# Kernel tuning notes

Hardware: AMD Instinct MI355X
Metric: run time of the kernel (lower is better)

The kernel has to match this reference:

```python
import jax, jax.numpy as jnp
import numpy as np

B, T, SLATE, D = 256, 16, 20, 256
N_ITEMS, N_USERS = 100000, 10000


def setup_inputs() -> dict:
    key = jax.random.key(0)
    ks = jax.random.split(key, 8)
    s = 1.0 / np.sqrt(D)  # PyTorch GRU/Linear init scale ~ U(-1/sqrt(H), 1/sqrt(H))
    return {
        "item_idxs": jax.random.randint(ks[0], (B, T, SLATE), 0, N_ITEMS),
        "user_idxs": jax.random.randint(ks[1], (B, T), 0, N_USERS),
        "responses": jnp.zeros((B, T, SLATE), jnp.float32),
        "item_table": jax.random.normal(ks[2], (N_ITEMS, D), jnp.float32) * 0.02,
        "user_table": jax.random.normal(ks[3], (N_USERS, D), jnp.float32) * 0.02,
        "W_ih": jax.random.uniform(ks[4], (3 * D, 2 * D), jnp.float32, -s, s),
        "W_hh": jax.random.uniform(ks[5], (3 * D, D), jnp.float32, -s, s),
        "b_ih": jnp.zeros((3 * D,), jnp.float32),
        "b_hh": jnp.zeros((3 * D,), jnp.float32),
        "W_out": jax.random.uniform(ks[6], (1, D), jnp.float32, -s, s),
        "b_out": jnp.zeros((1,), jnp.float32),
    }


def _gru_cell(x, h, W_ih, W_hh, b_ih, b_hh):
    # PyTorch GRUCell math. x: [N, 2D], h: [N, D]
    gi = x @ W_ih.T + b_ih  # [N, 3D]
    gh = h @ W_hh.T + b_hh  # [N, 3D]
    i_r, i_z, i_n = jnp.split(gi, 3, axis=-1)
    h_r, h_z, h_n = jnp.split(gh, 3, axis=-1)
    r = jax.nn.sigmoid(i_r + h_r)
    z = jax.nn.sigmoid(i_z + h_z)
    n = jnp.tanh(i_n + r * h_n)
    return (1.0 - z) * n + z * h


def reference(item_idxs, user_idxs, responses, item_table, user_table,
              W_ih, W_hh, b_ih, b_hh, W_out, b_out):
    # embedding lookup: item_embs [B,T,S,D], user_embs [B,T,D]
    item_embs = item_table[item_idxs]
    user_embs = user_table[user_idxs]
    N = B * T
    e = item_embs.reshape(N, SLATE, D).transpose(1, 0, 2)  # [S, N, D]
    h0 = user_embs.reshape(N, D)
    m0 = jnp.ones((N, 1), item_embs.dtype)  # 'soft' readout multiplier, 1 at step 0

    def step(carry, e_i):
        h, m = carry
        x = jnp.concatenate([e_i, e_i * m], axis=-1)  # [N, 2D]
        h = _gru_cell(x, h, W_ih, W_hh, b_ih, b_hh)
        y = h @ W_out.T + b_out  # [N, 1]
        return (h, jax.nn.sigmoid(y)), y[:, 0]

    _, ys = jax.lax.scan(step, (h0, m0), e)  # ys: [S, N]
    return ys.transpose(1, 0).reshape(B, T, SLATE)
```

## Files before the change

### kernel.cpp

```cpp
#include <hip/hip_runtime.h>
#include <math.h>

#define SLATE 20
#define DD 256
#define NSEQ 4096

typedef __attribute__((ext_vector_type(8))) short bf16x8;
typedef __attribute__((ext_vector_type(4))) float f32x4;
typedef unsigned short u16;
typedef unsigned int u32;

__device__ __forceinline__ u16 f2bf(float f) {
    unsigned u = __float_as_uint(f);
    u += 0x7fff + ((u >> 16) & 1);
    return (u16)(u >> 16);
}
__device__ __forceinline__ float blo(u32 u) { return __uint_as_float(u << 16); }
__device__ __forceinline__ float bhi(u32 u) { return __uint_as_float(u & 0xffff0000u); }
__device__ __forceinline__ float sigm_(float x) {
    return __builtin_amdgcn_rcpf(1.f + __builtin_amdgcn_exp2f(-1.44269504f * x));
}
__device__ __forceinline__ float tanh_(float x) {
    return 1.f - 2.f * __builtin_amdgcn_rcpf(1.f + __builtin_amdgcn_exp2f(2.88539008f * x));
}

__device__ __forceinline__ void gl_lds16(const void* g, void* l) {
    __builtin_amdgcn_global_load_lds(
        (const __attribute__((address_space(1))) unsigned int*)g,
        (__attribute__((address_space(3))) unsigned int*)l, 16, 0, 0);
}

__global__ void prep_w(const float* __restrict__ W_ih, const float* __restrict__ W_hh,
                       u16* __restrict__ W12, u16* __restrict__ Whh) {
    int i = blockIdx.x * 256 + threadIdx.x;
    if (i < 1536 * 256) {
        int j = i >> 8, k = i & 255;
        float v = (j < 768) ? W_ih[(size_t)j * 512 + k]
                            : W_ih[(size_t)(j - 768) * 512 + 256 + k];
        W12[i] = f2bf(v);
    } else {
        int i2 = i - 1536 * 256;
        Whh[i2] = f2bf(W_hh[i2]);
    }
}

__global__ void gather_e(int s0, const int* __restrict__ idxs, const float* __restrict__ itab,
                         u16* __restrict__ e_bf) {
    int g = blockIdx.x * 256 + threadIdx.x;
    int row = g >> 6, c = g & 63;
    int n = row & (NSEQ - 1), s = s0 + (row >> 12);
    int idx = idxs[n * SLATE + s];
    float4 v = *(const float4*)&itab[(size_t)idx * DD + c * 4];
    ushort4 o;
    o.x = f2bf(v.x); o.y = f2bf(v.y); o.z = f2bf(v.z); o.w = f2bf(v.w);
    *(ushort4*)&e_bf[(size_t)row * DD + c * 4] = o;
}

__global__ __launch_bounds__(256) void gemm_e(
        const u16* __restrict__ e_bf, const u16* __restrict__ W12,
        const float* __restrict__ b_ih, u16* __restrict__ Ge) {
    __shared__ u16 A_s[128][32];
    __shared__ u16 B_s[128][32];

    const int tid = threadIdx.x;
    const int w = tid >> 6, l = tid & 63, lm = l & 15, lq = l >> 4;
    const int wm = w & 1, wn = w >> 1;
    const size_t m0 = (size_t)blockIdx.y * 128;
    const size_t n0 = (size_t)blockIdx.x * 128;

    f32x4 acc[4][4];
    f32x4 zero4 = {0.f, 0.f, 0.f, 0.f};
#pragma unroll
    for (int mi = 0; mi < 4; ++mi)
#pragma unroll
        for (int nj = 0; nj < 4; ++nj) acc[mi][nj] = zero4;

    const int srow = w * 16 + (l >> 2);
    const int skc = (l & 3) * 8;
    const u16* gA = e_bf + (m0 + srow) * DD + skc;
    const u16* gB = W12 + (n0 + srow) * DD + skc;
    u16* lA = &A_s[0][0] + w * 512 + l * 8;
    u16* lB = &B_s[0][0] + w * 512 + l * 8;

    for (int kt = 0; kt < 8; ++kt) {
        const int ko = kt * 32;
        gl_lds16(gA + ko, lA);
        gl_lds16(gA + 64 * DD + ko, lA + 2048);
        gl_lds16(gB + ko, lB);
        gl_lds16(gB + 64 * DD + ko, lB + 2048);
        __syncthreads();
        bf16x8 af[4], bfr[4];
#pragma unroll
        for (int mi = 0; mi < 4; ++mi)
            af[mi] = *(const bf16x8*)&A_s[wm * 64 + mi * 16 + lm][lq * 8];
#pragma unroll
        for (int nj = 0; nj < 4; ++nj)
            bfr[nj] = *(const bf16x8*)&B_s[wn * 64 + nj * 16 + lm][lq * 8];
#pragma unroll
        for (int nj = 0; nj < 4; ++nj)
#pragma unroll
            for (int mi = 0; mi < 4; ++mi)
                acc[mi][nj] = __builtin_amdgcn_mfma_f32_16x16x32_bf16(af[mi], bfr[nj], acc[mi][nj], 0, 0, 0);
        __syncthreads();
    }
    float bb[4];
#pragma unroll
    for (int nj = 0; nj < 4; ++nj) {
        int col = (int)n0 + wn * 64 + nj * 16 + lm;
        bb[nj] = (col < 768) ? b_ih[col] : 0.f;
    }
#pragma unroll
    for (int mi = 0; mi < 4; ++mi)
#pragma unroll
        for (int rr = 0; rr < 4; ++rr) {
            u16* gp = Ge + (m0 + wm * 64 + mi * 16 + lq * 4 + rr) * 1536 + n0 + wn * 64 + lm;
#pragma unroll
            for (int nj = 0; nj < 4; ++nj) gp[nj * 16] = f2bf(acc[mi][nj][rr] + bb[nj]);
        }
}

__device__ __forceinline__ int hA_off(int seq, int kt, int lq2) {
    int v = ((kt & 3) << 2) | lq2;
    return kt * 512 + lq2 * 128 + ((seq ^ v) << 3);
}

__global__ __launch_bounds__(1024, 4) void seq_kernel(
        int s0, int C,
        const u16* __restrict__ Ge,
        const u16* __restrict__ Whh,
        const int* __restrict__ user_idxs, const float* __restrict__ user_table,
        const float* __restrict__ b_hh,
        const float* __restrict__ W_out, const float* __restrict__ b_out,
        float* __restrict__ h_g, float* __restrict__ m_g, float* __restrict__ out)
{
    __shared__ u16   hA[4096];
    __shared__ float gh_s[16][770];
    __shared__ u16   geL[2][16][1536];

    const int tid = threadIdx.x;
    const int w = tid >> 6, l = tid & 63, lm = l & 15, lq = l >> 4;
    const int n0 = blockIdx.x * 16;
    const int nw = n0 + w;
    const int jw = w * 48;

    const u16* wbase = Whh + (size_t)(jw + lm) * DD + lq * 8;
    bf16x8 warr0[8], warr1[8];
#pragma unroll
    for (int kt = 0; kt < 8; ++kt) {
        warr0[kt] = *(const bf16x8*)(wbase + kt * 32);
        warr1[kt] = *(const bf16x8*)(wbase + 16 * DD + kt * 32);
    }
    const u16* wb2 = wbase + 32 * DD;

    float bhh0 = b_hh[jw + lm], bhh1 = b_hh[jw + 16 + lm], bhh2 = b_hh[jw + 32 + lm];
    float2 woA = *(const float2*)&W_out[2 * l];
    float2 woB = *(const float2*)&W_out[2 * l + 128];
    const float bo = b_out[0];

    float h_reg[4]; float m_w;
    if (s0 == 0) {
        const float* hu = user_table + (size_t)user_idxs[nw] * DD;
        float2 a = *(const float2*)&hu[2 * l];
        float2 b = *(const float2*)&hu[2 * l + 128];
        h_reg[0] = a.x; h_reg[1] = a.y; h_reg[2] = b.x; h_reg[3] = b.y; m_w = 1.f;
    } else {
        float2 a = *(const float2*)&h_g[(size_t)nw * DD + 2 * l];
        float2 b = *(const float2*)&h_g[(size_t)nw * DD + 2 * l + 128];
        h_reg[0] = a.x; h_reg[1] = a.y; h_reg[2] = b.x; h_reg[3] = b.y; m_w = m_g[nw];
    }
#pragma unroll
    for (int c = 0; c < 2; ++c) {
        int kt = (l >> 4) + 4 * c, lq2 = (l >> 2) & 3;
        u32 pk = (u32)f2bf(h_reg[2 * c]) | ((u32)f2bf(h_reg[2 * c + 1]) << 16);
        *(u32*)&hA[hA_off(w, kt, lq2) + 2 * (l & 3)] = pk;
    }

    {
        const u16* g0 = Ge + ((size_t)0 * NSEQ + n0) * 1536;
        u16* l0 = &geL[0][0][0];
#pragma unroll
        for (int i = 0; i < 3; ++i) {
            int ii = w + 16 * i;
            gl_lds16(g0 + ii * 512 + l * 8, l0 + ii * 512);
        }
    }
    asm volatile("s_waitcnt lgkmcnt(0)" ::: "memory");
    __builtin_amdgcn_s_barrier();
    __builtin_amdgcn_sched_barrier(0);

    for (int sc = 0; sc < C; ++sc) {
        const int cur = sc & 1;

        f32x4 zero4 = {0.f, 0.f, 0.f, 0.f};
        f32x4 acc0 = zero4, acc1 = zero4, acc2 = zero4;
#pragma unroll
        for (int kt = 0; kt < 8; ++kt) {
            bf16x8 af = *(const bf16x8*)&hA[hA_off(lm, kt, lq)];
            acc0 = __builtin_amdgcn_mfma_f32_16x16x32_bf16(af, warr0[kt], acc0, 0, 0, 0);
            acc1 = __builtin_amdgcn_mfma_f32_16x16x32_bf16(af, warr1[kt], acc1, 0, 0, 0);
            bf16x8 b2 = *(const bf16x8*)(wb2 + kt * 32);
            acc2 = __builtin_amdgcn_mfma_f32_16x16x32_bf16(af, b2, acc2, 0, 0, 0);
        }

        __builtin_amdgcn_sched_barrier(0);
        if (sc + 1 < C) {
            const u16* gnx = Ge + ((size_t)(sc + 1) * NSEQ + n0) * 1536;
            u16* lnx = &geL[cur ^ 1][0][0];
#pragma unroll
            for (int i = 0; i < 3; ++i) {
                int ii = w + 16 * i;
                gl_lds16(gnx + ii * 512 + l * 8, lnx + ii * 512);
            }
        }

#pragma unroll
        for (int rr = 0; rr < 4; ++rr) {
            gh_s[lq * 4 + rr][jw + lm]      = acc0[rr] + bhh0;
            gh_s[lq * 4 + rr][jw + 16 + lm] = acc1[rr] + bhh1;
            gh_s[lq * 4 + rr][jw + 32 + lm] = acc2[rr] + bhh2;
        }
        asm volatile("s_waitcnt vmcnt(3) lgkmcnt(0)" ::: "memory");
        __builtin_amdgcn_s_barrier();
        __builtin_amdgcn_sched_barrier(0);

        const u32* grow = (const u32*)&geL[cur][w][0];
        u32 ge2[2][6];
#pragma unroll
        for (int c = 0; c < 2; ++c)
#pragma unroll
            for (int g = 0; g < 6; ++g)
                ge2[c][g] = grow[g * 128 + 64 * c + l];

        float yv = 0.f;
#pragma unroll
        for (int c = 0; c < 2; ++c) {
            const int d0 = 2 * l + 128 * c;
            float2 ghr = *(const float2*)&gh_s[w][d0];
            float2 ghz = *(const float2*)&gh_s[w][256 + d0];
            float2 ghn = *(const float2*)&gh_s[w][512 + d0];
            float ir_lo = fmaf(m_w, blo(ge2[c][3]), blo(ge2[c][0]));
            float ir_hi = fmaf(m_w, bhi(ge2[c][3]), bhi(ge2[c][0]));
            float iz_lo = fmaf(m_w, blo(ge2[c][4]), blo(ge2[c][1]));
            float iz_hi = fmaf(m_w, bhi(ge2[c][4]), bhi(ge2[c][1]));
            float in_lo = fmaf(m_w, blo(ge2[c][5]), blo(ge2[c][2]));
            float in_hi = fmaf(m_w, bhi(ge2[c][5]), bhi(ge2[c][2]));
            float r_lo = sigm_(ir_lo + ghr.x);
            float r_hi = sigm_(ir_hi + ghr.y);
            float z_lo = sigm_(iz_lo + ghz.x);
            float z_hi = sigm_(iz_hi + ghz.y);
            float n_lo = tanh_(fmaf(r_lo, ghn.x, in_lo));
            float n_hi = tanh_(fmaf(r_hi, ghn.y, in_hi));
            float hn_lo = fmaf(z_lo, h_reg[2 * c] - n_lo, n_lo);
            float hn_hi = fmaf(z_hi, h_reg[2 * c + 1] - n_hi, n_hi);
            h_reg[2 * c] = hn_lo; h_reg[2 * c + 1] = hn_hi;
            int kt = (l >> 4) + 4 * c, lq2 = (l >> 2) & 3;
            u32 pk = (u32)f2bf(hn_lo) | ((u32)f2bf(hn_hi) << 16);
            *(u32*)&hA[hA_off(w, kt, lq2) + 2 * (l & 3)] = pk;
            float2 wo2 = c ? woB : woA;
            yv += hn_lo * wo2.x + hn_hi * wo2.y;
        }
#pragma unroll
        for (int off = 32; off > 0; off >>= 1) yv += __shfl_xor(yv, off, 64);
        float y = yv + bo;
        if (l == 0) out[(size_t)nw * SLATE + (s0 + sc)] = y;
        m_w = sigm_(y);

        asm volatile("s_waitcnt lgkmcnt(0)" ::: "memory");
        __builtin_amdgcn_s_barrier();
        __builtin_amdgcn_sched_barrier(0);
    }

#pragma unroll
    for (int c = 0; c < 2; ++c) {
        float2 v; v.x = h_reg[2 * c]; v.y = h_reg[2 * c + 1];
        *(float2*)&h_g[(size_t)nw * DD + 2 * l + 128 * c] = v;
    }
    if (l == 0) m_g[nw] = m_w;
}

extern "C" void kernel_launch(void* const* d_in, const int* in_sizes, int n_in,
                              void* d_out, int out_size, void* d_ws, size_t ws_size,
                              hipStream_t stream) {
    const int*   item_idxs  = (const int*)d_in[0];
    const int*   user_idxs  = (const int*)d_in[1];
    const float* item_table = (const float*)d_in[3];
    const float* user_table = (const float*)d_in[4];
    const float* W_ih       = (const float*)d_in[5];
    const float* W_hh       = (const float*)d_in[6];
    const float* b_ih       = (const float*)d_in[7];
    const float* b_hh       = (const float*)d_in[8];
    const float* W_out      = (const float*)d_in[9];
    const float* b_out      = (const float*)d_in[10];
    float* out = (float*)d_out;

    const size_t fixed = 786432ull + 393216ull + 4194304ull + 16384ull;
    static const int cands[5] = {10, 5, 4, 2, 1};
    int C = 1;
    for (int i = 0; i < 5; ++i) {
        size_t need = (size_t)cands[i] * (12582912ull + 2097152ull) + fixed;
        if (need <= ws_size) { C = cands[i]; break; }
    }

    u16*   Ge   = (u16*)d_ws;
    u16*   e_bf = (u16*)((char*)d_ws + (size_t)C * 12582912ull);
    u16*   W12  = (u16*)((char*)e_bf + (size_t)C * 2097152ull);
    u16*   Whh  = (u16*)((char*)W12 + 786432ull);
    float* h_g  = (float*)((char*)Whh + 393216ull);
    float* m_g  = (float*)((char*)h_g + 4194304ull);

    prep_w<<<2304, 256, 0, stream>>>(W_ih, W_hh, W12, Whh);

    for (int s0 = 0; s0 < SLATE; s0 += C) {
        gather_e<<<C * 1024, 256, 0, stream>>>(s0, item_idxs, item_table, e_bf);
        dim3 gg(12, 32 * C);
        gemm_e<<<gg, 256, 0, stream>>>(e_bf, W12, b_ih, Ge);
        seq_kernel<<<256, 1024, 0, stream>>>(s0, C, Ge, Whh, user_idxs, user_table,
                                             b_hh, W_out, b_out, h_g, m_g, out);
    }
}
```

Baseline: 445.8 us.

## Halve seq_kernel block size, keep all W_hh fragments in registers, fold b_hh

The recurrent kernel now uses 512 threads, 8 waves, with each wave computing 96 gate columns and holding all six W_hh fragments in registers. Previously one third of W_hh was re-read from global memory every step. Each wave now processes two sequences using half-wave lanes, and the r/z parts of b_hh are folded into the precomputed input GEMM bias. The next-step Ge prefetch is issued earlier, before the MFMAs. The cost is much higher register pressure, about 192 VGPRs for weights, and fewer waves for the per-step elementwise work.

```diff
diff --git a/kernel.cpp b/kernel.cpp
--- a/kernel.cpp
+++ b/kernel.cpp
@@ -58,7 +58,8 @@
 
 __global__ __launch_bounds__(256) void gemm_e(
         const u16* __restrict__ e_bf, const u16* __restrict__ W12,
-        const float* __restrict__ b_ih, u16* __restrict__ Ge) {
+        const float* __restrict__ b_ih, const float* __restrict__ b_hh,
+        u16* __restrict__ Ge) {
     __shared__ u16 A_s[128][32];
     __shared__ u16 B_s[128][32];
 
@@ -107,7 +108,8 @@
 #pragma unroll
     for (int nj = 0; nj < 4; ++nj) {
         int col = (int)n0 + wn * 64 + nj * 16 + lm;
-        bb[nj] = (col < 768) ? b_ih[col] : 0.f;
+        bb[nj] = 0.f;
+        if (col < 768) bb[nj] = b_ih[col] + (col < 512 ? b_hh[col] : 0.f);
     }
 #pragma unroll
     for (int mi = 0; mi < 4; ++mi)
@@ -124,7 +126,7 @@
     return kt * 512 + lq2 * 128 + ((seq ^ v) << 3);
 }
 
-__global__ __launch_bounds__(1024, 4) void seq_kernel(
+__global__ __launch_bounds__(512, 2) void seq_kernel(
         int s0, int C,
         const u16* __restrict__ Ge,
         const u16* __restrict__ Whh,
@@ -139,50 +141,66 @@
 
     const int tid = threadIdx.x;
     const int w = tid >> 6, l = tid & 63, lm = l & 15, lq = l >> 4;
+    const int l5 = l & 31, sh = l >> 5;
     const int n0 = blockIdx.x * 16;
-    const int nw = n0 + w;
-    const int jw = w * 48;
-
-    const u16* wbase = Whh + (size_t)(jw + lm) * DD + lq * 8;
-    bf16x8 warr0[8], warr1[8];
-#pragma unroll
-    for (int kt = 0; kt < 8; ++kt) {
-        warr0[kt] = *(const bf16x8*)(wbase + kt * 32);
-        warr1[kt] = *(const bf16x8*)(wbase + 16 * DD + kt * 32);
-    }
-    const u16* wb2 = wbase + 32 * DD;
-
-    float bhh0 = b_hh[jw + lm], bhh1 = b_hh[jw + 16 + lm], bhh2 = b_hh[jw + 32 + lm];
-    float2 woA = *(const float2*)&W_out[2 * l];
-    float2 woB = *(const float2*)&W_out[2 * l + 128];
+    const int sloc = 2 * w + sh;
+    const int nw = n0 + sloc;
+    const int jw2 = w * 96;
+
+    bf16x8 warr[6][8];
+    const u16* wb = Whh + (size_t)(jw2 + lm) * DD + lq * 8;
+#pragma unroll
+    for (int fi = 0; fi < 6; ++fi)
+#pragma unroll
+        for (int kt = 0; kt < 8; ++kt)
+            warr[fi][kt] = *(const bf16x8*)(wb + fi * 16 * DD + kt * 32);
+
+    float bn[6];
+#pragma unroll
+    for (int fi = 0; fi < 6; ++fi) {
+        int colb = jw2 + fi * 16;
+        bn[fi] = (colb >= 512) ? b_hh[colb + lm] : 0.f;
+    }
+
+    float wo[8];
+#pragma unroll
+    for (int j = 0; j < 4; ++j) {
+        float2 t = *(const float2*)&W_out[2 * l5 + 64 * j];
+        wo[2 * j] = t.x; wo[2 * j + 1] = t.y;
+    }
     const float bo = b_out[0];
 
-    float h_reg[4]; float m_w;
+    float h_reg[8]; float m_w;
     if (s0 == 0) {
         const float* hu = user_table + (size_t)user_idxs[nw] * DD;
-        float2 a = *(const float2*)&hu[2 * l];
-        float2 b = *(const float2*)&hu[2 * l + 128];
-        h_reg[0] = a.x; h_reg[1] = a.y; h_reg[2] = b.x; h_reg[3] = b.y; m_w = 1.f;
+#pragma unroll
+        for (int j = 0; j < 4; ++j) {
+            float2 t = *(const float2*)&hu[2 * l5 + 64 * j];
+            h_reg[2 * j] = t.x; h_reg[2 * j + 1] = t.y;
+        }
+        m_w = 1.f;
     } else {
-        float2 a = *(const float2*)&h_g[(size_t)nw * DD + 2 * l];
-        float2 b = *(const float2*)&h_g[(size_t)nw * DD + 2 * l + 128];
-        h_reg[0] = a.x; h_reg[1] = a.y; h_reg[2] = b.x; h_reg[3] = b.y; m_w = m_g[nw];
-    }
-#pragma unroll
-    for (int c = 0; c < 2; ++c) {
-        int kt = (l >> 4) + 4 * c, lq2 = (l >> 2) & 3;
-        u32 pk = (u32)f2bf(h_reg[2 * c]) | ((u32)f2bf(h_reg[2 * c + 1]) << 16);
-        *(u32*)&hA[hA_off(w, kt, lq2) + 2 * (l & 3)] = pk;
+        const float* hp = h_g + (size_t)nw * DD;
+#pragma unroll
+        for (int j = 0; j < 4; ++j) {
+            float2 t = *(const float2*)&hp[2 * l5 + 64 * j];
+            h_reg[2 * j] = t.x; h_reg[2 * j + 1] = t.y;
+        }
+        m_w = m_g[nw];
+    }
+#pragma unroll
+    for (int j = 0; j < 4; ++j) {
+        int ktw = (l5 >> 4) + 2 * j, lq2 = (l5 & 15) >> 2;
+        u32 pk = (u32)f2bf(h_reg[2 * j]) | ((u32)f2bf(h_reg[2 * j + 1]) << 16);
+        *(u32*)&hA[hA_off(sloc, ktw, lq2) + 2 * (l5 & 3)] = pk;
     }
 
     {
-        const u16* g0 = Ge + ((size_t)0 * NSEQ + n0) * 1536;
+        const u16* g0 = Ge + (size_t)n0 * 1536;
         u16* l0 = &geL[0][0][0];
 #pragma unroll
-        for (int i = 0; i < 3; ++i) {
-            int ii = w + 16 * i;
-            gl_lds16(g0 + ii * 512 + l * 8, l0 + ii * 512);
-        }
+        for (int i = 0; i < 6; ++i)
+            gl_lds16(g0 + tid * 8 + i * 4096, l0 + tid * 8 + i * 4096);
     }
     asm volatile("s_waitcnt lgkmcnt(0)" ::: "memory");
     __builtin_amdgcn_s_barrier();
@@ -191,78 +209,75 @@
     for (int sc = 0; sc < C; ++sc) {
         const int cur = sc & 1;
 
+        if (sc + 1 < C) {
+            const u16* gn = Ge + ((size_t)(sc + 1) * NSEQ + n0) * 1536;
+            u16* ln = &geL[cur ^ 1][0][0];
+#pragma unroll
+            for (int i = 0; i < 6; ++i)
+                gl_lds16(gn + tid * 8 + i * 4096, ln + tid * 8 + i * 4096);
+        }
+        __builtin_amdgcn_sched_barrier(0);
+
         f32x4 zero4 = {0.f, 0.f, 0.f, 0.f};
-        f32x4 acc0 = zero4, acc1 = zero4, acc2 = zero4;
+        f32x4 acc[6];
+#pragma unroll
+        for (int fi = 0; fi < 6; ++fi) acc[fi] = zero4;
 #pragma unroll
         for (int kt = 0; kt < 8; ++kt) {
             bf16x8 af = *(const bf16x8*)&hA[hA_off(lm, kt, lq)];
-            acc0 = __builtin_amdgcn_mfma_f32_16x16x32_bf16(af, warr0[kt], acc0, 0, 0, 0);
-            acc1 = __builtin_amdgcn_mfma_f32_16x16x32_bf16(af, warr1[kt], acc1, 0, 0, 0);
-            bf16x8 b2 = *(const bf16x8*)(wb2 + kt * 32);
-            acc2 = __builtin_amdgcn_mfma_f32_16x16x32_bf16(af, b2, acc2, 0, 0, 0);
-        }
-
-        __builtin_amdgcn_sched_barrier(0);
-        if (sc + 1 < C) {
-            const u16* gnx = Ge + ((size_t)(sc + 1) * NSEQ + n0) * 1536;
-            u16* lnx = &geL[cur ^ 1][0][0];
-#pragma unroll
-            for (int i = 0; i < 3; ++i) {
-                int ii = w + 16 * i;
-                gl_lds16(gnx + ii * 512 + l * 8, lnx + ii * 512);
-            }
-        }
-
-#pragma unroll
-        for (int rr = 0; rr < 4; ++rr) {
-            gh_s[lq * 4 + rr][jw + lm]      = acc0[rr] + bhh0;
-            gh_s[lq * 4 + rr][jw + 16 + lm] = acc1[rr] + bhh1;
-            gh_s[lq * 4 + rr][jw + 32 + lm] = acc2[rr] + bhh2;
-        }
-        asm volatile("s_waitcnt vmcnt(3) lgkmcnt(0)" ::: "memory");
+#pragma unroll
+            for (int fi = 0; fi < 6; ++fi)
+                acc[fi] = __builtin_amdgcn_mfma_f32_16x16x32_bf16(af, warr[fi][kt], acc[fi], 0, 0, 0);
+        }
+#pragma unroll
+        for (int fi = 0; fi < 6; ++fi)
+#pragma unroll
+            for (int rr = 0; rr < 4; ++rr)
+                gh_s[lq * 4 + rr][jw2 + fi * 16 + lm] = acc[fi][rr] + bn[fi];
+
+        if (sc + 1 < C) { asm volatile("s_waitcnt vmcnt(6) lgkmcnt(0)" ::: "memory"); }
+        else            { asm volatile("s_waitcnt vmcnt(0) lgkmcnt(0)" ::: "memory"); }
         __builtin_amdgcn_s_barrier();
         __builtin_amdgcn_sched_barrier(0);
 
-        const u32* grow = (const u32*)&geL[cur][w][0];
-        u32 ge2[2][6];
-#pragma unroll
-        for (int c = 0; c < 2; ++c)
-#pragma unroll
-            for (int g = 0; g < 6; ++g)
-                ge2[c][g] = grow[g * 128 + 64 * c + l];
-
+        const u32* grow = (const u32*)&geL[cur][sloc][0];
         float yv = 0.f;
 #pragma unroll
-        for (int c = 0; c < 2; ++c) {
-            const int d0 = 2 * l + 128 * c;
-            float2 ghr = *(const float2*)&gh_s[w][d0];
-            float2 ghz = *(const float2*)&gh_s[w][256 + d0];
-            float2 ghn = *(const float2*)&gh_s[w][512 + d0];
-            float ir_lo = fmaf(m_w, blo(ge2[c][3]), blo(ge2[c][0]));
-            float ir_hi = fmaf(m_w, bhi(ge2[c][3]), bhi(ge2[c][0]));
-            float iz_lo = fmaf(m_w, blo(ge2[c][4]), blo(ge2[c][1]));
-            float iz_hi = fmaf(m_w, bhi(ge2[c][4]), bhi(ge2[c][1]));
-            float in_lo = fmaf(m_w, blo(ge2[c][5]), blo(ge2[c][2]));
-            float in_hi = fmaf(m_w, bhi(ge2[c][5]), bhi(ge2[c][2]));
+        for (int j = 0; j < 4; ++j) {
+            u32 g1r = grow[      l5 + 32 * j];
+            u32 g1z = grow[128 + l5 + 32 * j];
+            u32 g1n = grow[256 + l5 + 32 * j];
+            u32 g2r = grow[384 + l5 + 32 * j];
+            u32 g2z = grow[512 + l5 + 32 * j];
+            u32 g2n = grow[640 + l5 + 32 * j];
+            const int d0 = 2 * l5 + 64 * j;
+            float2 ghr = *(const float2*)&gh_s[sloc][d0];
+            float2 ghz = *(const float2*)&gh_s[sloc][256 + d0];
+            float2 ghn = *(const float2*)&gh_s[sloc][512 + d0];
+            float ir_lo = fmaf(m_w, blo(g2r), blo(g1r));
+            float ir_hi = fmaf(m_w, bhi(g2r), bhi(g1r));
+            float iz_lo = fmaf(m_w, blo(g2z), blo(g1z));
+            float iz_hi = fmaf(m_w, bhi(g2z), bhi(g1z));
+            float in_lo = fmaf(m_w, blo(g2n), blo(g1n));
+            float in_hi = fmaf(m_w, bhi(g2n), bhi(g1n));
             float r_lo = sigm_(ir_lo + ghr.x);
             float r_hi = sigm_(ir_hi + ghr.y);
             float z_lo = sigm_(iz_lo + ghz.x);
             float z_hi = sigm_(iz_hi + ghz.y);
             float n_lo = tanh_(fmaf(r_lo, ghn.x, in_lo));
             float n_hi = tanh_(fmaf(r_hi, ghn.y, in_hi));
-            float hn_lo = fmaf(z_lo, h_reg[2 * c] - n_lo, n_lo);
-            float hn_hi = fmaf(z_hi, h_reg[2 * c + 1] - n_hi, n_hi);
-            h_reg[2 * c] = hn_lo; h_reg[2 * c + 1] = hn_hi;
-            int kt = (l >> 4) + 4 * c, lq2 = (l >> 2) & 3;
+            float hn_lo = fmaf(z_lo, h_reg[2 * j] - n_lo, n_lo);
+            float hn_hi = fmaf(z_hi, h_reg[2 * j + 1] - n_hi, n_hi);
+            h_reg[2 * j] = hn_lo; h_reg[2 * j + 1] = hn_hi;
+            int ktw = (l5 >> 4) + 2 * j, lq2 = (l5 & 15) >> 2;
             u32 pk = (u32)f2bf(hn_lo) | ((u32)f2bf(hn_hi) << 16);
-            *(u32*)&hA[hA_off(w, kt, lq2) + 2 * (l & 3)] = pk;
-            float2 wo2 = c ? woB : woA;
-            yv += hn_lo * wo2.x + hn_hi * wo2.y;
-        }
-#pragma unroll
-        for (int off = 32; off > 0; off >>= 1) yv += __shfl_xor(yv, off, 64);
+            *(u32*)&hA[hA_off(sloc, ktw, lq2) + 2 * (l5 & 3)] = pk;
+            yv += hn_lo * wo[2 * j] + hn_hi * wo[2 * j + 1];
+        }
+#pragma unroll
+        for (int off = 16; off > 0; off >>= 1) yv += __shfl_xor(yv, off, 32);
         float y = yv + bo;
-        if (l == 0) out[(size_t)nw * SLATE + (s0 + sc)] = y;
+        if (l5 == 0) out[(size_t)nw * SLATE + (s0 + sc)] = y;
         m_w = sigm_(y);
 
         asm volatile("s_waitcnt lgkmcnt(0)" ::: "memory");
@@ -271,11 +286,11 @@
     }
 
 #pragma unroll
-    for (int c = 0; c < 2; ++c) {
-        float2 v; v.x = h_reg[2 * c]; v.y = h_reg[2 * c + 1];
-        *(float2*)&h_g[(size_t)nw * DD + 2 * l + 128 * c] = v;
-    }
-    if (l == 0) m_g[nw] = m_w;
+    for (int j = 0; j < 4; ++j) {
+        float2 v; v.x = h_reg[2 * j]; v.y = h_reg[2 * j + 1];
+        *(float2*)&h_g[(size_t)nw * DD + 2 * l5 + 64 * j] = v;
+    }
+    if (l5 == 0) m_g[nw] = m_w;
 }
 
 extern "C" void kernel_launch(void* const* d_in, const int* in_sizes, int n_in,
@@ -313,8 +328,8 @@
     for (int s0 = 0; s0 < SLATE; s0 += C) {
         gather_e<<<C * 1024, 256, 0, stream>>>(s0, item_idxs, item_table, e_bf);
         dim3 gg(12, 32 * C);
-        gemm_e<<<gg, 256, 0, stream>>>(e_bf, W12, b_ih, Ge);
-        seq_kernel<<<256, 1024, 0, stream>>>(s0, C, Ge, Whh, user_idxs, user_table,
-                                             b_hh, W_out, b_out, h_g, m_g, out);
-    }
-}
+        gemm_e<<<gg, 256, 0, stream>>>(e_bf, W12, b_ih, b_hh, Ge);
+        seq_kernel<<<256, 512, 0, stream>>>(s0, C, Ge, Whh, user_idxs, user_table,
+                                            b_hh, W_out, b_out, h_g, m_g, out);
+    }
+}
```

Measured after the change: 399.2 us. -10.5%, faster.
